# Optimization experiments

Hardware: AMD Instinct MI355X
Metric: run time of the kernel (lower is better)

The kernel has to match this reference:

```python
import jax, jax.numpy as jnp
from jax import lax
import numpy as np

B, M = 16384, 200            # flattened batch (B*TT), tokens per observation
NUM_LAYERS, GW, GH = 22, 11, 11
CNN_CH, HIDDEN = 128, 512
ACTION_NVEC = (9, 10)

MAX_VEC = jnp.array([9.0, 1.0, 1.0, 10.0, 3.0, 254.0, 1.0, 1.0, 235.0, 8.0, 9.0,
                     250.0, 29.0, 1.0, 1.0, 8.0, 1.0, 1.0, 6.0, 3.0, 1.0, 2.0],
                    jnp.float32)[None, :, None, None]  # [1,22,1,1]


def setup_inputs() -> dict:
    key = jax.random.key(0)
    ks = jax.random.split(key, 16)
    # compose coords byte so x,y nibbles are valid grid indices (0..10)
    xs = jax.random.randint(ks[0], (B, M), 0, GW)
    ys = jax.random.randint(ks[1], (B, M), 0, GH)
    coords = xs * 16 + ys
    atr = jax.random.randint(ks[2], (B, M), 0, NUM_LAYERS)
    val = jax.random.randint(ks[3], (B, M), 0, 11)
    observations = jnp.stack([coords, atr, val], axis=-1).astype(jnp.int32)  # [B,M,3]

    def nrm(k, shape, std=0.02):
        return (jax.random.normal(k, shape, jnp.float32) * std)

    return {
        "observations": observations,
        "conv1_w": nrm(ks[4], (CNN_CH, NUM_LAYERS, 5, 5)),
        "conv1_b": jnp.zeros((CNN_CH,), jnp.float32),
        "conv2_w": nrm(ks[5], (CNN_CH, CNN_CH, 3, 3)),
        "conv2_b": jnp.zeros((CNN_CH,), jnp.float32),
        "fc_w": nrm(ks[6], (HIDDEN // 2, CNN_CH)),
        "fc_b": jnp.zeros((HIDDEN // 2,), jnp.float32),
        "self_w": nrm(ks[7], (HIDDEN // 2, NUM_LAYERS)),
        "self_b": jnp.zeros((HIDDEN // 2,), jnp.float32),
        "actor0_w": nrm(ks[8], (ACTION_NVEC[0], HIDDEN), std=0.01),
        "actor0_b": jnp.zeros((ACTION_NVEC[0],), jnp.float32),
        "actor1_w": nrm(ks[9], (ACTION_NVEC[1], HIDDEN), std=0.01),
        "actor1_b": jnp.zeros((ACTION_NVEC[1],), jnp.float32),
        "value_w": nrm(ks[10], (1, HIDDEN)),
        "value_b": jnp.zeros((1,), jnp.float32),
    }


def reference(observations, conv1_w, conv1_b, conv2_w, conv2_b, fc_w, fc_b,
              self_w, self_b, actor0_w, actor0_b, actor1_w, actor1_b,
              value_w, value_b):
    obs = jnp.where(observations == 255, 0, observations)
    coords = obs[..., 0]
    xs = (coords >> 4) & 15
    ys = coords & 15
    atr = obs[..., 1]
    vals = obs[..., 2].astype(jnp.float32)           # [B,M]
    Bt = obs.shape[0]
    b_idx = jnp.broadcast_to(jnp.arange(Bt)[:, None], vals.shape)
    # masked scatter into dense grid (all tokens valid after 255->0 clamp)
    box = jnp.zeros((Bt, NUM_LAYERS, GW, GH), jnp.float32)
    box = box.at[b_idx, atr, xs, ys].set(vals, mode="drop")
    feats = box / MAX_VEC                            # [B,22,11,11]

    self_f = jax.nn.relu(feats[:, :, 5, 5] @ self_w.T + self_b)  # [B,256]

    dn = ("NCHW", "OIHW", "NCHW")
    h = lax.conv_general_dilated(feats, conv1_w, (3, 3), "VALID", dimension_numbers=dn)
    h = jax.nn.relu(h + conv1_b[None, :, None, None])            # [B,128,3,3]
    h = lax.conv_general_dilated(h, conv2_w, (1, 1), "VALID", dimension_numbers=dn)
    h = jax.nn.relu(h + conv2_b[None, :, None, None])            # [B,128,1,1]
    h = h.reshape(Bt, -1)
    cnn_f = jax.nn.relu(h @ fc_w.T + fc_b)                       # [B,256]

    hidden = jnp.concatenate([self_f, cnn_f], axis=1)            # [B,512]
    logits0 = hidden @ actor0_w.T + actor0_b
    logits1 = hidden @ actor1_w.T + actor1_b
    value = hidden @ value_w.T + value_b
    return (logits0, logits1, value)
```

## Files before the change

### kernel.cpp

```cpp
#include <hip/hip_runtime.h>

typedef unsigned short u16;
typedef __attribute__((ext_vector_type(8))) short short8;
typedef __attribute__((ext_vector_type(4))) float f32x4;

#define MFMA16(a, b, c) __builtin_amdgcn_mfma_f32_16x16x32_bf16((a), (b), (c), 0, 0, 0)

__device__ __forceinline__ u16 f2bf(float f) {
    unsigned u = __float_as_uint(f);
    unsigned r = (u + 0x7FFFu + ((u >> 16) & 1u)) >> 16;
    return (u16)r;
}

__device__ const float MAXV[22] = {9.f, 1.f, 1.f, 10.f, 3.f, 254.f, 1.f, 1.f, 235.f, 8.f, 9.f,
                                   250.f, 29.f, 1.f, 1.f, 8.f, 1.f, 1.f, 6.f, 3.f, 1.f, 2.f};

__global__ void prep_kernel(
    const float* c1w, const float* c1b, const float* c2w, const float* c2b,
    const float* fcw, const float* fcb, const float* sfw, const float* sfb,
    const float* a0w, const float* a0b, const float* a1w, const float* a1b,
    const float* vw, const float* vb,
    u16* W1F, u16* W2F, u16* FCF, u16* SELFF, u16* HEADF, float* BIAS)
{
    int idx = blockIdx.x * 256 + threadIdx.x;
    if (idx < 73728) {
        int grp = idx >> 9, off = idx & 511;
        int g = grp / 18, ks = grp - g * 18;
        int l = off >> 3, e = off & 7;
        int n = g * 16 + (l & 15);
        int k = ks * 32 + ((l >> 4) << 3) + e;
        float v = 0.f;
        if (k < 550) { int c = k / 25; v = c1w[n * 550 + k] * (1.0f / MAXV[c]); }
        W1F[idx] = f2bf(v);
    } else if (idx < 221184) {
        int j = idx - 73728;
        int grp = j >> 9, off = j & 511;
        int g = grp / 36, ks = grp - g * 36;
        int l = off >> 3, e = off & 7;
        int oc = g * 16 + (l & 15);
        int k = ks * 32 + ((l >> 4) << 3) + e;
        W2F[j] = f2bf(c2w[oc * 1152 + (k & 127) * 9 + (k >> 7)]);
    } else if (idx < 253952) {
        int j = idx - 221184;
        int grp = j >> 9, off = j & 511;
        int g = grp >> 2, kc = grp & 3;
        int l = off >> 3, e = off & 7;
        int n = g * 16 + (l & 15);
        int k = kc * 32 + ((l >> 4) << 3) + e;
        FCF[j] = f2bf(fcw[n * 128 + k]);
    } else if (idx < 262144) {
        int j = idx - 253952;
        int g = j >> 9, off = j & 511;
        int l = off >> 3, e = off & 7;
        int n = g * 16 + (l & 15);
        int k = ((l >> 4) << 3) + e;
        float v = (k < 22) ? sfw[n * 22 + k] * (1.0f / MAXV[k]) : 0.f;
        SELFF[j] = f2bf(v);
    } else if (idx < 278528) {
        int j = idx - 262144;
        int grp = j >> 9, off = j & 511;
        int g = grp >> 4, ks = grp & 15;
        int l = off >> 3, e = off & 7;
        int n = g * 16 + (l & 15);
        int k = ks * 32 + ((l >> 4) << 3) + e;
        float v = 0.f;
        if (n < 9) v = a0w[n * 512 + k];
        else if (n < 19) v = a1w[(n - 9) * 512 + k];
        else if (n == 19) v = vw[k];
        HEADF[j] = f2bf(v);
    } else if (idx < 279328) {
        int j = idx - 278528;
        float v = 0.f;
        if (j < 128) v = c1b[j];
        else if (j < 256) v = c2b[j - 128];
        else if (j < 512) v = fcb[j - 256];
        else if (j < 768) v = sfb[j - 512];
        else {
            int j2 = j - 768;
            if (j2 < 9) v = a0b[j2]; else if (j2 < 19) v = a1b[j2 - 9]; else if (j2 == 19) v = vb[0];
        }
        BIAS[j] = v;
    }
}

__global__ __launch_bounds__(256, 3) void k12_kernel(
    const int* __restrict__ obs, const u16* __restrict__ W1F,
    const float* __restrict__ BIAS, u16* __restrict__ h1F, u16* __restrict__ s22g)
{
    __shared__ __align__(16) u16 A[36 * 576];
    __shared__ __align__(16) int box[2664];
    __shared__ u16 s22[128];
    const int tid = threadIdx.x, w = tid >> 6, l = tid & 63;
    const int s0 = blockIdx.x * 4;

    int tok[4][3];
    if (tid < 200) {
        #pragma unroll
        for (int p = 0; p < 4; ++p) {
            const int* tp = obs + (long)(s0 + p) * 600 + tid * 3;
            tok[p][0] = tp[0]; tok[p][1] = tp[1]; tok[p][2] = tp[2];
        }
    }

    {
        short8 z = {0, 0, 0, 0, 0, 0, 0, 0};
        for (int i = tid; i < 2592; i += 256) *(short8*)(A + i * 8) = z;
        int4 zz = {0, 0, 0, 0};
        for (int i = tid; i < 666; i += 256) ((int4*)box)[i] = zz;
        if (tid < 128) s22[tid] = 0;
    }
    __syncthreads();

    #pragma unroll
    for (int p = 0; p < 4; ++p) {
        int ce = 0, en = 0, va = 0, xa = 0, ya = 0, aa = 0, ok = 0;
        if (tid < 200) {
            int c = tok[p][0], a = tok[p][1], v = tok[p][2];
            c = (c == 255) ? 0 : c; a = (a == 255) ? 0 : a; v = (v == 255) ? 0 : v;
            int xs = (c >> 4) & 15, ys = c & 15;
            ok = ((unsigned)a < 22u) & (xs < 11) & (ys < 11);
            ce = a * 121 + xs * 11 + ys;
            en = ((p + 1) << 16) | (tid << 8) | (v & 255);
            va = v; xa = xs; ya = ys; aa = a;
            if (ok) atomicMax(&box[ce], en);
        }
        __syncthreads();
        if (ok && box[ce] == en) {
            u16 bv = f2bf((float)va);
            if (xa == 5 && ya == 5) s22[p * 32 + aa] = bv;
            int bcol = aa * 25;
            #pragma unroll
            for (int ox = 0; ox < 3; ++ox) {
                int kx = xa - 3 * ox;
                if ((unsigned)kx > 4u) continue;
                #pragma unroll
                for (int oy = 0; oy < 3; ++oy) {
                    int ky = ya - 3 * oy;
                    if ((unsigned)ky > 4u) continue;
                    int row = p * 9 + ox * 3 + oy;
                    int byte = ((row * 576 + bcol + kx * 5 + ky) << 1) ^ ((row & 7) << 4);
                    *(u16*)((char*)A + byte) = bv;
                }
            }
        }
        __syncthreads();
    }
    if (tid < 128) s22g[s0 * 32 + tid] = s22[tid];

    int Aoff[3][2];
    #pragma unroll
    for (int mt = 0; mt < 3; ++mt) {
        int row = mt * 16 + (l & 15);
        row = row < 36 ? row : 35;
        int koff = (l >> 4) << 3;
        Aoff[mt][0] = ((row * 576 + koff) << 1) ^ ((row & 7) << 4);
        Aoff[mt][1] = ((row * 576 + 32 + koff) << 1) ^ ((row & 7) << 4);
    }
    const u16* Wp0 = W1F + ((w * 2 + 0) * 18 << 9) + l * 8;
    const u16* Wp1 = W1F + ((w * 2 + 1) * 18 << 9) + l * 8;

    f32x4 acc[3][2];
    const f32x4 fz = {0.f, 0.f, 0.f, 0.f};
    #pragma unroll
    for (int i = 0; i < 3; ++i) { acc[i][0] = fz; acc[i][1] = fz; }

    short8 cb0 = *(const short8*)(Wp0);
    short8 cb1 = *(const short8*)(Wp1);
    short8 nb0 = *(const short8*)(Wp0 + 512);
    short8 nb1 = *(const short8*)(Wp1 + 512);
    __builtin_amdgcn_s_setprio(1);
    #pragma unroll
    for (int ks = 0; ks < 18; ++ks) {
        short8 t0 = cb0, t1 = cb1;
        if (ks < 16) {
            t0 = *(const short8*)(Wp0 + (ks + 2) * 512);
            t1 = *(const short8*)(Wp1 + (ks + 2) * 512);
        }
        short8 a0 = *(const short8*)((const char*)A + Aoff[0][ks & 1] + (ks >> 1) * 128);
        short8 a1 = *(const short8*)((const char*)A + Aoff[1][ks & 1] + (ks >> 1) * 128);
        short8 a2 = *(const short8*)((const char*)A + Aoff[2][ks & 1] + (ks >> 1) * 128);
        acc[0][0] = MFMA16(a0, cb0, acc[0][0]);
        acc[0][1] = MFMA16(a0, cb1, acc[0][1]);
        acc[1][0] = MFMA16(a1, cb0, acc[1][0]);
        acc[1][1] = MFMA16(a1, cb1, acc[1][1]);
        acc[2][0] = MFMA16(a2, cb0, acc[2][0]);
        acc[2][1] = MFMA16(a2, cb1, acc[2][1]);
        cb0 = nb0; cb1 = nb1; nb0 = t0; nb1 = t1;
    }
    __builtin_amdgcn_s_setprio(0);

    u16* R = (u16*)box;
    #pragma unroll
    for (int mt = 0; mt < 3; ++mt) {
        #pragma unroll
        for (int nt = 0; nt < 2; ++nt) {
            int col = w * 32 + nt * 16 + (l & 15);
            float bias = BIAS[col];
            int hif = nt * 2 + ((l & 15) >> 3);
            int ef = l & 7;
            #pragma unroll
            for (int r = 0; r < 4; ++r) {
                int row = mt * 16 + ((l >> 4) << 2) + r;
                if (row < 36) {
                    int ds = row / 9;
                    int pos = row - ds * 9;
                    int ks = pos * 4 + w;
                    float v = acc[mt][nt][r] + bias;
                    v = v > 0.f ? v : 0.f;
                    R[(ks * 16 + hif * 4 + ds) * 8 + ef] = f2bf(v);
                }
            }
        }
    }
    __syncthreads();
    {
        const long Cbase = (long)(s0 >> 4) * 18432 + (s0 & 15) * 8;
        #pragma unroll
        for (int q = 0; q < 3; ++q) {
            int slot = tid + q * 256;
            if (slot < 576) {
                int ks = slot >> 4, lf = slot & 15;
                *(short8*)(h1F + Cbase + ks * 512 + (lf >> 2) * 128 + (lf & 3) * 8) =
                    *(const short8*)(R + slot * 8);
            }
        }
    }
}

__global__ __launch_bounds__(256, 2) void k3a_kernel(
    const u16* __restrict__ h1F, const u16* __restrict__ W2F,
    const float* __restrict__ BIAS, u16* __restrict__ a3F)
{
    const int tid = threadIdx.x, w = tid >> 6, l = tid & 63;
    const int sb = blockIdx.x * 2, s0 = blockIdx.x * 32;
    const float* c2b = BIAS + 128;
    const f32x4 fz = {0.f, 0.f, 0.f, 0.f};
    f32x4 acc[2][2];
    acc[0][0] = fz; acc[0][1] = fz; acc[1][0] = fz; acc[1][1] = fz;

    const u16* A0p = h1F + (long)(sb + 0) * 18432 + l * 8;
    const u16* A1p = h1F + (long)(sb + 1) * 18432 + l * 8;
    const u16* B0p = W2F + ((w * 2 + 0) * 36 << 9) + l * 8;
    const u16* B1p = W2F + ((w * 2 + 1) * 36 << 9) + l * 8;

    short8 ca0 = *(const short8*)(A0p), ca1 = *(const short8*)(A1p);
    short8 cb0 = *(const short8*)(B0p), cb1 = *(const short8*)(B1p);
    short8 na0 = *(const short8*)(A0p + 512), na1 = *(const short8*)(A1p + 512);
    short8 nb0 = *(const short8*)(B0p + 512), nb1 = *(const short8*)(B1p + 512);
    __builtin_amdgcn_s_setprio(1);
    #pragma unroll
    for (int ks = 0; ks < 36; ++ks) {
        short8 t0 = ca0, t1 = ca1, t2 = cb0, t3 = cb1;
        if (ks < 34) {
            t0 = *(const short8*)(A0p + (ks + 2) * 512);
            t1 = *(const short8*)(A1p + (ks + 2) * 512);
            t2 = *(const short8*)(B0p + (ks + 2) * 512);
            t3 = *(const short8*)(B1p + (ks + 2) * 512);
        }
        acc[0][0] = MFMA16(ca0, cb0, acc[0][0]);
        acc[0][1] = MFMA16(ca0, cb1, acc[0][1]);
        acc[1][0] = MFMA16(ca1, cb0, acc[1][0]);
        acc[1][1] = MFMA16(ca1, cb1, acc[1][1]);
        ca0 = na0; ca1 = na1; cb0 = nb0; cb1 = nb1;
        na0 = t0; na1 = t1; nb0 = t2; nb1 = t3;
    }
    __builtin_amdgcn_s_setprio(0);

    #pragma unroll
    for (int mt = 0; mt < 2; ++mt) {
        #pragma unroll
        for (int nt = 0; nt < 2; ++nt) {
            int col = w * 32 + nt * 16 + (l & 15);
            float bias = c2b[col];
            #pragma unroll
            for (int r = 0; r < 4; ++r) {
                int row = mt * 16 + ((l >> 4) << 2) + r;
                int s = s0 + row;
                float v = acc[mt][nt][r] + bias; v = v > 0.f ? v : 0.f;
                long ad = (long)(s >> 4) * 2048 + (col >> 5) * 512 +
                          (s & 15) * 8 + (((col >> 3) & 3) << 7) + (col & 7);
                a3F[ad] = f2bf(v);
            }
        }
    }
}

__global__ __launch_bounds__(256, 4) void k3b_kernel(
    const u16* __restrict__ a3F, const u16* __restrict__ s22g,
    const u16* __restrict__ FCF, const u16* __restrict__ SELFF,
    const u16* __restrict__ HEADF, const float* __restrict__ BIAS,
    float* __restrict__ out, int B)
{
    __shared__ __align__(16) u16 HID[16 * 520];
    const int tid = threadIdx.x, w = tid >> 6, l = tid & 63;
    const int s0 = blockIdx.x * 16;
    const float* fcb = BIAS + 256;
    const float* sfb = BIAS + 512;
    const float* hdb = BIAS + 768;
    const f32x4 fz = {0.f, 0.f, 0.f, 0.f};

    f32x4 acc8[4];
    #pragma unroll
    for (int j = 0; j < 4; ++j) acc8[j] = fz;
    #pragma unroll
    for (int kc = 0; kc < 4; ++kc) {
        short8 a = *(const short8*)(a3F + (long)blockIdx.x * 2048 + kc * 512 + l * 8);
        #pragma unroll
        for (int nt = 0; nt < 4; ++nt) {
            short8 bf = *(const short8*)(FCF + (((w * 4 + nt) * 4 + kc) << 9) + l * 8);
            acc8[nt] = MFMA16(a, bf, acc8[nt]);
        }
    }
    #pragma unroll
    for (int nt = 0; nt < 4; ++nt) {
        int col = w * 64 + nt * 16 + (l & 15);
        float bias = fcb[col];
        #pragma unroll
        for (int r = 0; r < 4; ++r) {
            int row = ((l >> 4) << 2) + r;
            float v = acc8[nt][r] + bias; v = v > 0.f ? v : 0.f;
            HID[row * 520 + 256 + col] = f2bf(v);
        }
    }

    {
        f32x4 acc9[4];
        #pragma unroll
        for (int j = 0; j < 4; ++j) acc9[j] = fz;
        short8 a = *(const short8*)(s22g + (s0 + (l & 15)) * 32 + ((l >> 4) << 3));
        #pragma unroll
        for (int nt = 0; nt < 4; ++nt) {
            short8 bs = *(const short8*)(SELFF + ((w * 4 + nt) << 9) + l * 8);
            acc9[nt] = MFMA16(a, bs, acc9[nt]);
        }
        #pragma unroll
        for (int nt = 0; nt < 4; ++nt) {
            int col = w * 64 + nt * 16 + (l & 15);
            float bias = sfb[col];
            #pragma unroll
            for (int r = 0; r < 4; ++r) {
                int row = ((l >> 4) << 2) + r;
                float v = acc9[nt][r] + bias; v = v > 0.f ? v : 0.f;
                HID[row * 520 + col] = f2bf(v);
            }
        }
    }
    __syncthreads();

    if (w < 2) {
        f32x4 hacc = fz;
        #pragma unroll
        for (int ks = 0; ks < 16; ++ks) {
            short8 a = *(const short8*)(HID + (l & 15) * 520 + ks * 32 + ((l >> 4) << 3));
            short8 b = *(const short8*)(HEADF + ((w * 16 + ks) << 9) + l * 8);
            hacc = MFMA16(a, b, hacc);
        }
        #pragma unroll
        for (int r = 0; r < 4; ++r) {
            int srow = s0 + ((l >> 4) << 2) + r;
            int col = w * 16 + (l & 15);
            float v = hacc[r] + hdb[col];
            if (col < 9) out[(long)srow * 9 + col] = v;
            else if (col < 19) out[(long)B * 9 + (long)srow * 10 + (col - 9)] = v;
            else if (col == 19) out[(long)B * 19 + srow] = v;
        }
    }
}

extern "C" void kernel_launch(void* const* d_in, const int* in_sizes, int n_in,
                              void* d_out, int out_size, void* d_ws, size_t ws_size,
                              hipStream_t stream)
{
    const int*   obs = (const int*)d_in[0];
    const float* c1w = (const float*)d_in[1];
    const float* c1b = (const float*)d_in[2];
    const float* c2w = (const float*)d_in[3];
    const float* c2b = (const float*)d_in[4];
    const float* fcw = (const float*)d_in[5];
    const float* fcb = (const float*)d_in[6];
    const float* sfw = (const float*)d_in[7];
    const float* sfb = (const float*)d_in[8];
    const float* a0w = (const float*)d_in[9];
    const float* a0b = (const float*)d_in[10];
    const float* a1w = (const float*)d_in[11];
    const float* a1b = (const float*)d_in[12];
    const float* vw  = (const float*)d_in[13];
    const float* vb  = (const float*)d_in[14];
    const int B = in_sizes[0] / 600;

    char* ws = (char*)d_ws;
    u16*   W1F   = (u16*)(ws + 0);
    u16*   W2F   = (u16*)(ws + 147456);
    u16*   FCF   = (u16*)(ws + 442368);
    u16*   SELFF = (u16*)(ws + 507904);
    u16*   HEADF = (u16*)(ws + 524288);
    float* BIAS  = (float*)(ws + 557056);
    u16*   s22g  = (u16*)(ws + 560256);
    u16*   h1F   = (u16*)(ws + 560256 + (size_t)B * 64);
    u16*   a3F   = (u16*)(ws + 560256 + (size_t)B * 64 + (size_t)B * 2304);

    prep_kernel<<<1092, 256, 0, stream>>>(c1w, c1b, c2w, c2b, fcw, fcb, sfw, sfb,
                                          a0w, a0b, a1w, a1b, vw, vb,
                                          W1F, W2F, FCF, SELFF, HEADF, BIAS);
    k12_kernel<<<B / 4, 256, 0, stream>>>(obs, W1F, BIAS, h1F, s22g);
    k3a_kernel<<<B / 32, 256, 0, stream>>>(h1F, W2F, BIAS, a3F);
    k3b_kernel<<<B / 16, 256, 0, stream>>>(a3F, s22g, FCF, SELFF, HEADF, BIAS,
                                           (float*)d_out, B);
}
```

Measured before the change: 79.22 us.

## Give each wave its own sample's scatter and drop the atomic dedup box

Each wavefront now loads and scatters the 200 tokens of one sample into its own slice of the im2col buffer. Previously all 256 threads handled four samples in turn, with an LDS atomicMax box to pick one winner per duplicate cell and block-wide barriers between phases. Dropping the box frees LDS, and the conv1 output staging now reuses the A buffer behind an added barrier. This removes most block barriers and the atomics, but duplicate cells are now resolved by plain last-writer LDS stores inside a wave, so the result is less deterministic when several lanes write the same cell.

```diff
diff --git a/kernel.cpp b/kernel.cpp
--- a/kernel.cpp
+++ b/kernel.cpp
@@ -88,64 +88,54 @@
     const float* __restrict__ BIAS, u16* __restrict__ h1F, u16* __restrict__ s22g)
 {
     __shared__ __align__(16) u16 A[36 * 576];
-    __shared__ __align__(16) int box[2664];
     __shared__ u16 s22[128];
     const int tid = threadIdx.x, w = tid >> 6, l = tid & 63;
     const int s0 = blockIdx.x * 4;
 
-    int tok[4][3];
-    if (tid < 200) {
-        #pragma unroll
-        for (int p = 0; p < 4; ++p) {
-            const int* tp = obs + (long)(s0 + p) * 600 + tid * 3;
-            tok[p][0] = tp[0]; tok[p][1] = tp[1]; tok[p][2] = tp[2];
-        }
+    const int* myobs = obs + (long)(s0 + w) * 600;
+    int tk[4][3];
+    #pragma unroll
+    for (int r = 0; r < 4; ++r) {
+        int m = r * 64 + l; int mm = m < 200 ? m : 0;
+        tk[r][0] = myobs[mm * 3]; tk[r][1] = myobs[mm * 3 + 1]; tk[r][2] = myobs[mm * 3 + 2];
     }
 
     {
         short8 z = {0, 0, 0, 0, 0, 0, 0, 0};
-        for (int i = tid; i < 2592; i += 256) *(short8*)(A + i * 8) = z;
-        int4 zz = {0, 0, 0, 0};
-        for (int i = tid; i < 666; i += 256) ((int4*)box)[i] = zz;
-        if (tid < 128) s22[tid] = 0;
-    }
-    __syncthreads();
-
-    #pragma unroll
-    for (int p = 0; p < 4; ++p) {
-        int ce = 0, en = 0, va = 0, xa = 0, ya = 0, aa = 0, ok = 0;
-        if (tid < 200) {
-            int c = tok[p][0], a = tok[p][1], v = tok[p][2];
-            c = (c == 255) ? 0 : c; a = (a == 255) ? 0 : a; v = (v == 255) ? 0 : v;
-            int xs = (c >> 4) & 15, ys = c & 15;
-            ok = ((unsigned)a < 22u) & (xs < 11) & (ys < 11);
-            ce = a * 121 + xs * 11 + ys;
-            en = ((p + 1) << 16) | (tid << 8) | (v & 255);
-            va = v; xa = xs; ya = ys; aa = a;
-            if (ok) atomicMax(&box[ce], en);
-        }
-        __syncthreads();
-        if (ok && box[ce] == en) {
-            u16 bv = f2bf((float)va);
-            if (xa == 5 && ya == 5) s22[p * 32 + aa] = bv;
-            int bcol = aa * 25;
+        for (int i = l; i < 648; i += 64) *(short8*)(A + w * 5184 + i * 8) = z;
+        if (l < 32) s22[w * 32 + l] = 0;
+    }
+    __builtin_amdgcn_sched_barrier(0);
+
+    #pragma unroll
+    for (int r = 0; r < 4; ++r) {
+        int m = r * 64 + l;
+        int c = tk[r][0], a = tk[r][1], v = tk[r][2];
+        c = (c == 255) ? 0 : c; a = (a == 255) ? 0 : a; v = (v == 255) ? 0 : v;
+        int xs = (c >> 4) & 15, ys = c & 15;
+        int ok = (m < 200) & ((unsigned)a < 22u) & (xs < 11) & (ys < 11);
+        if (ok) {
+            u16 bv = f2bf((float)v);
+            if (xs == 5 && ys == 5) s22[w * 32 + a] = bv;
+            int bcol = a * 25;
             #pragma unroll
             for (int ox = 0; ox < 3; ++ox) {
-                int kx = xa - 3 * ox;
+                int kx = xs - 3 * ox;
                 if ((unsigned)kx > 4u) continue;
                 #pragma unroll
                 for (int oy = 0; oy < 3; ++oy) {
-                    int ky = ya - 3 * oy;
+                    int ky = ys - 3 * oy;
                     if ((unsigned)ky > 4u) continue;
-                    int row = p * 9 + ox * 3 + oy;
+                    int row = w * 9 + ox * 3 + oy;
                     int byte = ((row * 576 + bcol + kx * 5 + ky) << 1) ^ ((row & 7) << 4);
                     *(u16*)((char*)A + byte) = bv;
                 }
             }
         }
-        __syncthreads();
-    }
-    if (tid < 128) s22g[s0 * 32 + tid] = s22[tid];
+        __builtin_amdgcn_sched_barrier(0);
+    }
+    if (l < 32) s22g[(s0 + w) * 32 + l] = s22[w * 32 + l];
+    __syncthreads();
 
     int Aoff[3][2];
     #pragma unroll
@@ -188,8 +178,9 @@
         cb0 = nb0; cb1 = nb1; nb0 = t0; nb1 = t1;
     }
     __builtin_amdgcn_s_setprio(0);
-
-    u16* R = (u16*)box;
+    __syncthreads();
+
+    u16* R = (u16*)A;
     #pragma unroll
     for (int mt = 0; mt < 3; ++mt) {
         #pragma unroll
```

Result: no change. 77.68 us (-1.9%).
